# Kernel optimization log

Measured on AMD Instinct MI355X. Metric: run time of the kernel, lower is better.

The kernel has to match this reference:

```python
import jax, jax.numpy as jnp
import numpy as np

EMBED = 1024
HEADS = 16
HEAD_DIM = EMBED // HEADS


def setup_inputs() -> dict:
    key = jax.random.key(0)
    ks = jax.random.split(key, 11)
    B, L, D = 2, 2048, EMBED
    s = 0.02
    return {
        "q": jax.random.normal(ks[0], (B, L, D), jnp.float32),
        "k": jax.random.normal(ks[1], (B, L, D), jnp.float32),
        "v": jax.random.normal(ks[2], (B, L, D), jnp.float32),
        "w_q": jax.random.normal(ks[3], (D, D), jnp.float32) * s,
        "b_q": jnp.zeros((D,), jnp.float32),
        "w_k": jax.random.normal(ks[4], (D, D), jnp.float32) * s,
        "b_k": jnp.zeros((D,), jnp.float32),
        "w_v": jax.random.normal(ks[5], (D, D), jnp.float32) * s,
        "b_v": jnp.zeros((D,), jnp.float32),
        "w_o": jax.random.normal(ks[6], (D, D), jnp.float32) * s,
        "b_o": jnp.zeros((D,), jnp.float32),
    }


def reference(q, k, v, w_q, b_q, w_k, b_k, w_v, b_v, w_o, b_o):
    B, L, D = q.shape
    H, Dh = HEADS, HEAD_DIM
    # Linear projections (torch Linear: x @ W.T + b)
    qp = (q @ w_q.T + b_q).reshape(B, L, H, Dh)
    kp = (k @ w_k.T + b_k).reshape(B, L, H, Dh)
    vp = (v @ w_v.T + b_v).reshape(B, L, H, Dh)
    # energy: [n, h, q, k]
    energy = jnp.einsum("nqhd,nkhd->nhqk", qp, kp)
    scale = 1.0 / jnp.sqrt(jnp.asarray(Dh, qp.dtype))
    attn = jax.nn.softmax(energy * scale, axis=-1)
    ctx = jnp.einsum("nhql,nlhd->nqhd", attn, vp).reshape(B, L, D)
    return ctx @ w_o.T + b_o
```

## Files before the change

### kernel.cpp

```cpp
#include <hip/hip_runtime.h>

typedef __bf16 bf16;
typedef __bf16 bf16x4 __attribute__((ext_vector_type(4)));
typedef __bf16 bf16x8 __attribute__((ext_vector_type(8)));
typedef float f32x4 __attribute__((ext_vector_type(4)));

#define MFMA16(a, b, c) __builtin_amdgcn_mfma_f32_16x16x32_bf16((a), (b), (c), 0, 0, 0)

#define QSCALE 0.18033688011112042f

__device__ inline void gld16(const void* g, void* l) {
    __builtin_amdgcn_global_load_lds(
        (const __attribute__((address_space(1))) unsigned int*)g,
        (__attribute__((address_space(3))) unsigned int*)l, 16, 0, 0);
}

__device__ inline bf16x8 cvt8(float4 a, float4 b) {
    bf16x8 v;
    v[0] = (bf16)a.x; v[1] = (bf16)a.y; v[2] = (bf16)a.z; v[3] = (bf16)a.w;
    v[4] = (bf16)b.x; v[5] = (bf16)b.y; v[6] = (bf16)b.z; v[7] = (bf16)b.w;
    return v;
}

__global__ __launch_bounds__(256) void cvt3_kernel(
    const float* __restrict__ s0, bf16* __restrict__ d0,
    const float* __restrict__ s1, bf16* __restrict__ d1,
    const float* __restrict__ s2, bf16* __restrict__ d2)
{
    const float* src = blockIdx.y == 0 ? s0 : blockIdx.y == 1 ? s1 : s2;
    bf16*        dst = blockIdx.y == 0 ? d0 : blockIdx.y == 1 ? d1 : d2;
    int i = (blockIdx.x * 256 + threadIdx.x) * 8;
    float4 a = *(const float4*)&src[i];
    float4 b = *(const float4*)&src[i + 4];
    *(bf16x8*)&dst[i] = cvt8(a, b);
}

__global__ __launch_bounds__(256) void cvt_kernel(
    const float* __restrict__ src, bf16* __restrict__ dst, int n)
{
    int i = (blockIdx.x * 256 + threadIdx.x) * 8;
    if (i < n) {
        float4 a = *(const float4*)&src[i];
        float4 b = *(const float4*)&src[i + 4];
        *(bf16x8*)&dst[i] = cvt8(a, b);
    }
}

__global__ __launch_bounds__(256) void qkv_gemm(
    const float* __restrict__ q, const float* __restrict__ k,
    const float* __restrict__ v,
    const bf16* __restrict__ wq, const float* __restrict__ bq,
    const bf16* __restrict__ wk, const float* __restrict__ bk,
    const bf16* __restrict__ wv, const float* __restrict__ bv,
    bf16* __restrict__ Qp, bf16* __restrict__ Kp, bf16* __restrict__ Vt)
{
    __shared__ __align__(16) bf16 sm[8192 + 2 * 8192];
    bf16* As = sm;
    bf16* Bs = sm + 8192;
    bf16* Ts = sm;

    const int id  = blockIdx.x;
    const int pr  = (id >> 6) * 8 + (id & 7);
    const int proj = pr >> 5;
    const int m0  = (pr & 31) * 128;
    const int n0  = ((id >> 3) & 7) * 128;

    const float* A    = proj == 0 ? q  : proj == 1 ? k  : v;
    const bf16*  B    = proj == 0 ? wq : proj == 1 ? wk : wv;
    const float* bias = proj == 0 ? bq : proj == 1 ? bk : bv;

    const int tid  = threadIdx.x;
    const int lane = tid & 63;
    const int w    = tid >> 6;
    const int g    = lane >> 4;
    const int ln   = lane & 15;
    const int rowb = (w & 1) * 64;
    const int colb = (w >> 1) * 64;
    const int srow = tid >> 3, slc = tid & 7;
    const int ro   = lane >> 3, lc = lane & 7;

    float4 ra[4][2];
    for (int i = 0; i < 4; ++i) {
        const float* p = &A[(size_t)(m0 + srow + 32 * i) * 1024 + slc * 8];
        ra[i][0] = *(const float4*)p;
        ra[i][1] = *(const float4*)(p + 4);
    }
    for (int j = 0; j < 4; ++j) {
        int base = w * 32 + j * 8;
        int row  = base + ro;
        int c    = lc ^ (row & 7);
        gld16(&B[(size_t)(n0 + row) * 1024 + c * 8], &Bs[base * 64]);
    }

    f32x4 acc[4][4] = {};

    for (int t = 0; t < 16; ++t) {
        __syncthreads();
        for (int i = 0; i < 4; ++i) {
            int row = srow + 32 * i;
            *(bf16x8*)&As[row * 64 + (slc ^ (row & 7)) * 8] = cvt8(ra[i][0], ra[i][1]);
        }
        __syncthreads();
        if (t < 15) {
            int k1 = (t + 1) * 64;
            for (int i = 0; i < 4; ++i) {
                const float* p = &A[(size_t)(m0 + srow + 32 * i) * 1024 + k1 + slc * 8];
                ra[i][0] = *(const float4*)p;
                ra[i][1] = *(const float4*)(p + 4);
            }
            int bsel = (t + 1) & 1;
            for (int j = 0; j < 4; ++j) {
                int base = w * 32 + j * 8;
                int row  = base + ro;
                int c    = lc ^ (row & 7);
                gld16(&B[(size_t)(n0 + row) * 1024 + k1 + c * 8],
                      &Bs[bsel * 8192 + base * 64]);
            }
        }
        const bf16* Bt = Bs + (t & 1) * 8192;
        for (int ks = 0; ks < 2; ++ks) {
            bf16x8 af[4], bfm[4];
            for (int mi = 0; mi < 4; ++mi) {
                int row = rowb + mi * 16 + ln;
                af[mi] = *(const bf16x8*)&As[row * 64 + ((ks * 4 + g) ^ (ln & 7)) * 8];
            }
            for (int ni = 0; ni < 4; ++ni) {
                int row = colb + ni * 16 + ln;
                bfm[ni] = *(const bf16x8*)&Bt[row * 64 + ((ks * 4 + g) ^ (ln & 7)) * 8];
            }
            for (int mi = 0; mi < 4; ++mi)
                for (int ni = 0; ni < 4; ++ni)
                    acc[mi][ni] = MFMA16(af[mi], bfm[ni], acc[mi][ni]);
        }
    }

    if (proj != 2) {
        for (int mi = 0; mi < 4; ++mi) {
            for (int ni = 0; ni < 4; ++ni) {
                int col = n0 + colb + ni * 16 + ln;
                float bv_ = bias[col];
                int rowbase = m0 + rowb + mi * 16 + g * 4;
                if (proj == 0) {
                    for (int r = 0; r < 4; ++r)
                        Qp[(size_t)(rowbase + r) * 1024 + col] =
                            (bf16)((acc[mi][ni][r] + bv_) * QSCALE);
                } else {
                    for (int r = 0; r < 4; ++r)
                        Kp[(size_t)(rowbase + r) * 1024 + col] =
                            (bf16)(acc[mi][ni][r] + bv_);
                }
            }
        }
    } else {
        __syncthreads();
        for (int mi = 0; mi < 4; ++mi) {
            for (int ni = 0; ni < 4; ++ni) {
                int col = colb + ni * 16 + ln;
                float bv_ = bias[n0 + col];
                int row = rowb + mi * 16 + g * 4;
                bf16x4 pk;
                for (int r = 0; r < 4; ++r) pk[r] = (bf16)(acc[mi][ni][r] + bv_);
                *(bf16x4*)&Ts[col * 132 + row] = pk;
            }
        }
        __syncthreads();
        const int bidx = m0 >> 11;
        const int tok0 = m0 & 2047;
        for (int i = 0; i < 8; ++i) {
            int c    = tid + 256 * i;
            int col  = c >> 4;
            int t64  = (c >> 3) & 1;
            int cc   = c & 7;
            int gcol = n0 + col;
            union { bf16 e[8]; uint4 u; } tmp;
            for (int j = 0; j < 8; ++j) {
                int s = 2 * cc + (j >> 2) + ((j & 3) << 4);
                tmp.e[j] = Ts[col * 132 + t64 * 64 + s];
            }
            size_t dst = ((size_t)(bidx * 16 + (gcol >> 6)) * 64 + (gcol & 63)) * 2048
                         + tok0 + t64 * 64 + cc * 8;
            *(uint4*)&Vt[dst] = tmp.u;
        }
    }
}

__global__ __launch_bounds__(256) void gemm_out(
    const bf16* __restrict__ A, const bf16* __restrict__ B,
    const float* __restrict__ bias, float* __restrict__ C)
{
    __shared__ __align__(16) bf16 sm[2 * 4096 + 2 * 8192];
    bf16* As = sm;
    bf16* Bs = sm + 8192;

    const int id = blockIdx.x;
    const int m0 = ((id >> 6) * 8 + (id & 7)) * 64;
    const int n0 = ((id >> 3) & 7) * 128;

    const int tid  = threadIdx.x;
    const int lane = tid & 63;
    const int w    = tid >> 6;
    const int g    = lane >> 4;
    const int ln   = lane & 15;
    const int rowb = (w & 1) * 32;
    const int colb = (w >> 1) * 64;
    const int ro   = lane >> 3, lc = lane & 7;

    auto issue = [&](int t) {
        int k0 = t * 64, sel = t & 1;
        for (int j = 0; j < 2; ++j) {
            int base = w * 16 + j * 8;
            int row  = base + ro;
            int c    = lc ^ (row & 7);
            gld16(&A[(size_t)(m0 + row) * 1024 + k0 + c * 8],
                  &As[sel * 4096 + base * 64]);
        }
        for (int j = 0; j < 4; ++j) {
            int base = w * 32 + j * 8;
            int row  = base + ro;
            int c    = lc ^ (row & 7);
            gld16(&B[(size_t)(n0 + row) * 1024 + k0 + c * 8],
                  &Bs[sel * 8192 + base * 64]);
        }
    };

    issue(0);
    f32x4 acc[2][4] = {};

    for (int t = 0; t < 16; ++t) {
        __syncthreads();
        if (t < 15) issue(t + 1);
        const bf16* At = As + (t & 1) * 4096;
        const bf16* Bt = Bs + (t & 1) * 8192;
        for (int ks = 0; ks < 2; ++ks) {
            bf16x8 af[2], bfm[4];
            for (int mi = 0; mi < 2; ++mi) {
                int row = rowb + mi * 16 + ln;
                af[mi] = *(const bf16x8*)&At[row * 64 + ((ks * 4 + g) ^ (ln & 7)) * 8];
            }
            for (int ni = 0; ni < 4; ++ni) {
                int row = colb + ni * 16 + ln;
                bfm[ni] = *(const bf16x8*)&Bt[row * 64 + ((ks * 4 + g) ^ (ln & 7)) * 8];
            }
            for (int mi = 0; mi < 2; ++mi)
                for (int ni = 0; ni < 4; ++ni)
                    acc[mi][ni] = MFMA16(af[mi], bfm[ni], acc[mi][ni]);
        }
    }

    for (int mi = 0; mi < 2; ++mi) {
        for (int ni = 0; ni < 4; ++ni) {
            int col = n0 + colb + ni * 16 + ln;
            float bv_ = bias[col];
            int rowbase = m0 + rowb + mi * 16 + g * 4;
            for (int r = 0; r < 4; ++r)
                C[(size_t)(rowbase + r) * 1024 + col] = acc[mi][ni][r] + bv_;
        }
    }
}

__global__ __launch_bounds__(256) void attn_kernel(
    const bf16* __restrict__ Qp, const bf16* __restrict__ Kp,
    const bf16* __restrict__ Vt, bf16* __restrict__ Ctx)
{
    __shared__ __align__(16) bf16 smem[8192 + 2 * 4096 + 2 * 4096];
    bf16* Ps = smem;
    bf16* Qs = smem;
    bf16* Ks = smem + 8192;
    bf16* Vs = smem + 16384;

    const int id = blockIdx.x;
    const int qt = (id >> 3) & 15;
    const int bh = (id >> 7) * 8 + (id & 7);

    const int tid  = threadIdx.x;
    const int lane = tid & 63;
    const int w    = tid >> 6;
    const int g    = lane >> 4;
    const int ln   = lane & 15;
    const int ro   = lane >> 3, lc = lane & 7;
    const size_t rowQ0 = (size_t)(bh >> 4) * 2048 + qt * 128;
    const size_t rowK0 = (size_t)(bh >> 4) * 2048;
    const int hcol = (bh & 15) * 64;
    const bf16* VtB = Vt + (size_t)bh * 64 * 2048;

    for (int j = 0; j < 4; ++j) {
        int base = w * 32 + j * 8;
        int row  = base + ro;
        int c    = lc ^ (row & 7);
        gld16(&Qp[(rowQ0 + row) * 1024 + hcol + c * 8], &Qs[base * 64]);
    }
    for (int j = 0; j < 2; ++j) {
        int base = w * 16 + j * 8;
        int kv   = base + ro;
        int c    = lc ^ (kv & 7);
        gld16(&Kp[(rowK0 + kv) * 1024 + hcol + c * 8], &Ks[base * 64]);
        gld16(&VtB[(size_t)kv * 2048 + c * 8], &Vs[base * 64]);
    }
    __syncthreads();

    bf16x8 qf[2][2];
    for (int mi = 0; mi < 2; ++mi)
        for (int ks = 0; ks < 2; ++ks) {
            int row = w * 32 + mi * 16 + ln;
            qf[mi][ks] = *(const bf16x8*)&Qs[row * 64 + ((ks * 4 + g) ^ (ln & 7)) * 8];
        }

    f32x4 oacc[2][4] = {};
    float l_part[2][4] = {};

    for (int t = 0; t < 32; ++t) {
        if (t < 31) {
            int sel = (t + 1) & 1, kvo = (t + 1) * 64;
            for (int j = 0; j < 2; ++j) {
                int base = w * 16 + j * 8;
                int kv   = base + ro;
                int c    = lc ^ (kv & 7);
                gld16(&Kp[(rowK0 + kvo + kv) * 1024 + hcol + c * 8],
                      &Ks[sel * 4096 + base * 64]);
                gld16(&VtB[(size_t)kv * 2048 + kvo + c * 8],
                      &Vs[sel * 4096 + base * 64]);
            }
        }
        const bf16* Kt = Ks + (t & 1) * 4096;
        const bf16* Vti = Vs + (t & 1) * 4096;

        f32x4 sf[2][4] = {};
        for (int ks = 0; ks < 2; ++ks) {
            bf16x8 kf[4];
            for (int nj = 0; nj < 4; ++nj) {
                int row = nj * 16 + ln;
                kf[nj] = *(const bf16x8*)&Kt[row * 64 + ((ks * 4 + g) ^ (ln & 7)) * 8];
            }
            for (int mi = 0; mi < 2; ++mi)
                for (int nj = 0; nj < 4; ++nj)
                    sf[mi][nj] = MFMA16(qf[mi][ks], kf[nj], sf[mi][nj]);
        }

        for (int mi = 0; mi < 2; ++mi) {
            for (int r = 0; r < 4; ++r) {
                float p0 = __builtin_amdgcn_exp2f(sf[mi][0][r]);
                float p1 = __builtin_amdgcn_exp2f(sf[mi][1][r]);
                float p2 = __builtin_amdgcn_exp2f(sf[mi][2][r]);
                float p3 = __builtin_amdgcn_exp2f(sf[mi][3][r]);
                l_part[mi][r] += (p0 + p1) + (p2 + p3);
                int qrow = w * 32 + mi * 16 + g * 4 + r;
                int slot = ln ^ ((qrow & 7) << 1);
                bf16x4 pk;
                pk[0] = (bf16)p0; pk[1] = (bf16)p1; pk[2] = (bf16)p2; pk[3] = (bf16)p3;
                *(bf16x4*)&Ps[qrow * 64 + slot * 4] = pk;
            }
        }

        for (int ks = 0; ks < 2; ++ks) {
            bf16x8 pf[2], vf[4];
            for (int mi = 0; mi < 2; ++mi) {
                int row = w * 32 + mi * 16 + ln;
                int p = (ks * 8 + g * 2) ^ ((row & 7) << 1);
                pf[mi] = *(const bf16x8*)&Ps[row * 64 + p * 4];
            }
            for (int nd = 0; nd < 4; ++nd) {
                int row = nd * 16 + ln;
                vf[nd] = *(const bf16x8*)&Vti[row * 64 + ((ks * 4 + g) ^ (ln & 7)) * 8];
            }
            for (int mi = 0; mi < 2; ++mi)
                for (int nd = 0; nd < 4; ++nd)
                    oacc[mi][nd] = MFMA16(pf[mi], vf[nd], oacc[mi][nd]);
        }
        __syncthreads();
    }

    for (int mi = 0; mi < 2; ++mi) {
        for (int r = 0; r < 4; ++r) {
            float l = l_part[mi][r];
            for (int off = 8; off >= 1; off >>= 1)
                l += __shfl_xor(l, off, 64);
            float inv = 1.0f / l;
            size_t row = rowQ0 + w * 32 + mi * 16 + g * 4 + r;
            for (int nd = 0; nd < 4; ++nd)
                Ctx[row * 1024 + hcol + nd * 16 + ln] = (bf16)(oacc[mi][nd][r] * inv);
        }
    }
}

extern "C" void kernel_launch(void* const* d_in, const int* in_sizes, int n_in,
                              void* d_out, int out_size, void* d_ws, size_t ws_size,
                              hipStream_t stream)
{
    const float* q  = (const float*)d_in[0];
    const float* k  = (const float*)d_in[1];
    const float* v  = (const float*)d_in[2];
    const float* wq = (const float*)d_in[3];
    const float* bq = (const float*)d_in[4];
    const float* wk = (const float*)d_in[5];
    const float* bk = (const float*)d_in[6];
    const float* wv = (const float*)d_in[7];
    const float* bv = (const float*)d_in[8];
    const float* wo = (const float*)d_in[9];
    const float* bo = (const float*)d_in[10];
    float* out = (float*)d_out;

    const int M = 4096, D = 1024;
    bf16* Qp = (bf16*)d_ws;
    bf16* Kp = Qp + (size_t)M * D;
    bf16* Vt = Kp + (size_t)M * D;
    bf16* Ctx = Qp;
    bf16* wob = Kp;

    bf16* wqb = (bf16*)d_out;
    bf16* wkb = wqb + (size_t)D * D;
    bf16* wvb = wkb + (size_t)D * D;

    cvt3_kernel<<<dim3(512, 3), 256, 0, stream>>>(wq, wqb, wk, wkb, wv, wvb);
    qkv_gemm<<<768, 256, 0, stream>>>(q, k, v, wqb, bq, wkb, bk, wvb, bv,
                                      Qp, Kp, Vt);
    attn_kernel<<<512, 256, 0, stream>>>(Qp, Kp, Vt, Ctx);
    cvt_kernel<<<512, 256, 0, stream>>>(wo, wob, D * D);
    gemm_out<<<512, 256, 0, stream>>>(Ctx, wob, bo, out);
}
```

Baseline: 239.0 us.

## Pre-convert activations to bf16, load QKV tiles via LDS DMA, halve attention q-tile

Adds a single conversion kernel that turns q, k, v and all four weights into bf16 up front. A new QKV GEMM can then stream both operands straight into LDS with global_load_lds instead of converting fp32 in registers. The attention kernel now uses 64-row query tiles across 1024 blocks instead of 128-row tiles across 512, for more parallelism and less shared memory per block. The fast path runs only if the workspace is at least 40 MB, otherwise it falls back to the old sequence. The new GEMM drops double-buffering and waits on each stage, and the extra conversion pass adds memory traffic.

```diff
diff --git a/kernel.cpp b/kernel.cpp
--- a/kernel.cpp
+++ b/kernel.cpp
@@ -20,6 +20,33 @@
     v[0] = (bf16)a.x; v[1] = (bf16)a.y; v[2] = (bf16)a.z; v[3] = (bf16)a.w;
     v[4] = (bf16)b.x; v[5] = (bf16)b.y; v[6] = (bf16)b.z; v[7] = (bf16)b.w;
     return v;
+}
+
+__global__ __launch_bounds__(256) void cvt7_kernel(
+    const float* __restrict__ q,  bf16* __restrict__ qb,
+    const float* __restrict__ k,  bf16* __restrict__ kb,
+    const float* __restrict__ v,  bf16* __restrict__ vb,
+    const float* __restrict__ wq, bf16* __restrict__ wqb,
+    const float* __restrict__ wk, bf16* __restrict__ wkb,
+    const float* __restrict__ wv, bf16* __restrict__ wvb,
+    const float* __restrict__ wo, bf16* __restrict__ wob)
+{
+    const float* src; bf16* dst; int n;
+    switch (blockIdx.y) {
+        case 0: src = q;  dst = qb;  n = 1 << 22; break;
+        case 1: src = k;  dst = kb;  n = 1 << 22; break;
+        case 2: src = v;  dst = vb;  n = 1 << 22; break;
+        case 3: src = wq; dst = wqb; n = 1 << 20; break;
+        case 4: src = wk; dst = wkb; n = 1 << 20; break;
+        case 5: src = wv; dst = wvb; n = 1 << 20; break;
+        default: src = wo; dst = wob; n = 1 << 20; break;
+    }
+    int i = (blockIdx.x * 256 + threadIdx.x) * 8;
+    if (i < n) {
+        float4 a = *(const float4*)&src[i];
+        float4 b = *(const float4*)&src[i + 4];
+        *(bf16x8*)&dst[i] = cvt8(a, b);
+    }
 }
 
 __global__ __launch_bounds__(256) void cvt3_kernel(
@@ -46,15 +73,15 @@
     }
 }
 
-__global__ __launch_bounds__(256) void qkv_gemm(
-    const float* __restrict__ q, const float* __restrict__ k,
-    const float* __restrict__ v,
+__global__ __launch_bounds__(256) void qkv_bf16(
+    const bf16* __restrict__ qb, const bf16* __restrict__ kb,
+    const bf16* __restrict__ vb,
     const bf16* __restrict__ wq, const float* __restrict__ bq,
     const bf16* __restrict__ wk, const float* __restrict__ bk,
     const bf16* __restrict__ wv, const float* __restrict__ bv,
     bf16* __restrict__ Qp, bf16* __restrict__ Kp, bf16* __restrict__ Vt)
 {
-    __shared__ __align__(16) bf16 sm[8192 + 2 * 8192];
+    __shared__ __align__(16) bf16 sm[16896];
     bf16* As = sm;
     bf16* Bs = sm + 8192;
     bf16* Ts = sm;
@@ -65,7 +92,7 @@
     const int m0  = (pr & 31) * 128;
     const int n0  = ((id >> 3) & 7) * 128;
 
-    const float* A    = proj == 0 ? q  : proj == 1 ? k  : v;
+    const bf16*  A    = proj == 0 ? qb : proj == 1 ? kb : vb;
     const bf16*  B    = proj == 0 ? wq : proj == 1 ? wk : wv;
     const float* bias = proj == 0 ? bq : proj == 1 ? bk : bv;
 
@@ -76,48 +103,24 @@
     const int ln   = lane & 15;
     const int rowb = (w & 1) * 64;
     const int colb = (w >> 1) * 64;
-    const int srow = tid >> 3, slc = tid & 7;
     const int ro   = lane >> 3, lc = lane & 7;
 
-    float4 ra[4][2];
-    for (int i = 0; i < 4; ++i) {
-        const float* p = &A[(size_t)(m0 + srow + 32 * i) * 1024 + slc * 8];
-        ra[i][0] = *(const float4*)p;
-        ra[i][1] = *(const float4*)(p + 4);
-    }
-    for (int j = 0; j < 4; ++j) {
-        int base = w * 32 + j * 8;
-        int row  = base + ro;
-        int c    = lc ^ (row & 7);
-        gld16(&B[(size_t)(n0 + row) * 1024 + c * 8], &Bs[base * 64]);
-    }
-
+    auto issue = [&](int t) {
+        int k0 = t * 64;
+        for (int j = 0; j < 4; ++j) {
+            int base = w * 32 + j * 8;
+            int row  = base + ro;
+            int c    = lc ^ (row & 7);
+            gld16(&A[(size_t)(m0 + row) * 1024 + k0 + c * 8], &As[base * 64]);
+            gld16(&B[(size_t)(n0 + row) * 1024 + k0 + c * 8], &Bs[base * 64]);
+        }
+    };
+
+    issue(0);
     f32x4 acc[4][4] = {};
 
     for (int t = 0; t < 16; ++t) {
         __syncthreads();
-        for (int i = 0; i < 4; ++i) {
-            int row = srow + 32 * i;
-            *(bf16x8*)&As[row * 64 + (slc ^ (row & 7)) * 8] = cvt8(ra[i][0], ra[i][1]);
-        }
-        __syncthreads();
-        if (t < 15) {
-            int k1 = (t + 1) * 64;
-            for (int i = 0; i < 4; ++i) {
-                const float* p = &A[(size_t)(m0 + srow + 32 * i) * 1024 + k1 + slc * 8];
-                ra[i][0] = *(const float4*)p;
-                ra[i][1] = *(const float4*)(p + 4);
-            }
-            int bsel = (t + 1) & 1;
-            for (int j = 0; j < 4; ++j) {
-                int base = w * 32 + j * 8;
-                int row  = base + ro;
-                int c    = lc ^ (row & 7);
-                gld16(&B[(size_t)(n0 + row) * 1024 + k1 + c * 8],
-                      &Bs[bsel * 8192 + base * 64]);
-            }
-        }
-        const bf16* Bt = Bs + (t & 1) * 8192;
         for (int ks = 0; ks < 2; ++ks) {
             bf16x8 af[4], bfm[4];
             for (int mi = 0; mi < 4; ++mi) {
@@ -126,12 +129,14 @@
             }
             for (int ni = 0; ni < 4; ++ni) {
                 int row = colb + ni * 16 + ln;
-                bfm[ni] = *(const bf16x8*)&Bt[row * 64 + ((ks * 4 + g) ^ (ln & 7)) * 8];
+                bfm[ni] = *(const bf16x8*)&Bs[row * 64 + ((ks * 4 + g) ^ (ln & 7)) * 8];
             }
             for (int mi = 0; mi < 4; ++mi)
                 for (int ni = 0; ni < 4; ++ni)
                     acc[mi][ni] = MFMA16(af[mi], bfm[ni], acc[mi][ni]);
         }
+        __syncthreads();
+        if (t < 15) issue(t + 1);
     }
 
     if (proj != 2) {
@@ -152,7 +157,6 @@
             }
         }
     } else {
-        __syncthreads();
         for (int mi = 0; mi < 4; ++mi) {
             for (int ni = 0; ni < 4; ++ni) {
                 int col = colb + ni * 16 + ln;
@@ -184,6 +188,144 @@
     }
 }
 
+__global__ __launch_bounds__(256) void qkv_gemm(
+    const float* __restrict__ q, const float* __restrict__ k,
+    const float* __restrict__ v,
+    const bf16* __restrict__ wq, const float* __restrict__ bq,
+    const bf16* __restrict__ wk, const float* __restrict__ bk,
+    const bf16* __restrict__ wv, const float* __restrict__ bv,
+    bf16* __restrict__ Qp, bf16* __restrict__ Kp, bf16* __restrict__ Vt)
+{
+    __shared__ __align__(16) bf16 sm[8192 + 2 * 8192];
+    bf16* As = sm;
+    bf16* Bs = sm + 8192;
+    bf16* Ts = sm;
+
+    const int id  = blockIdx.x;
+    const int pr  = (id >> 6) * 8 + (id & 7);
+    const int proj = pr >> 5;
+    const int m0  = (pr & 31) * 128;
+    const int n0  = ((id >> 3) & 7) * 128;
+
+    const float* A    = proj == 0 ? q  : proj == 1 ? k  : v;
+    const bf16*  B    = proj == 0 ? wq : proj == 1 ? wk : wv;
+    const float* bias = proj == 0 ? bq : proj == 1 ? bk : bv;
+
+    const int tid  = threadIdx.x;
+    const int lane = tid & 63;
+    const int w    = tid >> 6;
+    const int g    = lane >> 4;
+    const int ln   = lane & 15;
+    const int rowb = (w & 1) * 64;
+    const int colb = (w >> 1) * 64;
+    const int srow = tid >> 3, slc = tid & 7;
+    const int ro   = lane >> 3, lc = lane & 7;
+
+    float4 ra[4][2];
+    for (int i = 0; i < 4; ++i) {
+        const float* p = &A[(size_t)(m0 + srow + 32 * i) * 1024 + slc * 8];
+        ra[i][0] = *(const float4*)p;
+        ra[i][1] = *(const float4*)(p + 4);
+    }
+    for (int j = 0; j < 4; ++j) {
+        int base = w * 32 + j * 8;
+        int row  = base + ro;
+        int c    = lc ^ (row & 7);
+        gld16(&B[(size_t)(n0 + row) * 1024 + c * 8], &Bs[base * 64]);
+    }
+
+    f32x4 acc[4][4] = {};
+
+    for (int t = 0; t < 16; ++t) {
+        __syncthreads();
+        for (int i = 0; i < 4; ++i) {
+            int row = srow + 32 * i;
+            *(bf16x8*)&As[row * 64 + (slc ^ (row & 7)) * 8] = cvt8(ra[i][0], ra[i][1]);
+        }
+        __syncthreads();
+        if (t < 15) {
+            int k1 = (t + 1) * 64;
+            for (int i = 0; i < 4; ++i) {
+                const float* p = &A[(size_t)(m0 + srow + 32 * i) * 1024 + k1 + slc * 8];
+                ra[i][0] = *(const float4*)p;
+                ra[i][1] = *(const float4*)(p + 4);
+            }
+            int bsel = (t + 1) & 1;
+            for (int j = 0; j < 4; ++j) {
+                int base = w * 32 + j * 8;
+                int row  = base + ro;
+                int c    = lc ^ (row & 7);
+                gld16(&B[(size_t)(n0 + row) * 1024 + k1 + c * 8],
+                      &Bs[bsel * 8192 + base * 64]);
+            }
+        }
+        const bf16* Bt = Bs + (t & 1) * 8192;
+        for (int ks = 0; ks < 2; ++ks) {
+            bf16x8 af[4], bfm[4];
+            for (int mi = 0; mi < 4; ++mi) {
+                int row = rowb + mi * 16 + ln;
+                af[mi] = *(const bf16x8*)&As[row * 64 + ((ks * 4 + g) ^ (ln & 7)) * 8];
+            }
+            for (int ni = 0; ni < 4; ++ni) {
+                int row = colb + ni * 16 + ln;
+                bfm[ni] = *(const bf16x8*)&Bt[row * 64 + ((ks * 4 + g) ^ (ln & 7)) * 8];
+            }
+            for (int mi = 0; mi < 4; ++mi)
+                for (int ni = 0; ni < 4; ++ni)
+                    acc[mi][ni] = MFMA16(af[mi], bfm[ni], acc[mi][ni]);
+        }
+    }
+
+    if (proj != 2) {
+        for (int mi = 0; mi < 4; ++mi) {
+            for (int ni = 0; ni < 4; ++ni) {
+                int col = n0 + colb + ni * 16 + ln;
+                float bv_ = bias[col];
+                int rowbase = m0 + rowb + mi * 16 + g * 4;
+                if (proj == 0) {
+                    for (int r = 0; r < 4; ++r)
+                        Qp[(size_t)(rowbase + r) * 1024 + col] =
+                            (bf16)((acc[mi][ni][r] + bv_) * QSCALE);
+                } else {
+                    for (int r = 0; r < 4; ++r)
+                        Kp[(size_t)(rowbase + r) * 1024 + col] =
+                            (bf16)(acc[mi][ni][r] + bv_);
+                }
+            }
+        }
+    } else {
+        __syncthreads();
+        for (int mi = 0; mi < 4; ++mi) {
+            for (int ni = 0; ni < 4; ++ni) {
+                int col = colb + ni * 16 + ln;
+                float bv_ = bias[n0 + col];
+                int row = rowb + mi * 16 + g * 4;
+                bf16x4 pk;
+                for (int r = 0; r < 4; ++r) pk[r] = (bf16)(acc[mi][ni][r] + bv_);
+                *(bf16x4*)&Ts[col * 132 + row] = pk;
+            }
+        }
+        __syncthreads();
+        const int bidx = m0 >> 11;
+        const int tok0 = m0 & 2047;
+        for (int i = 0; i < 8; ++i) {
+            int c    = tid + 256 * i;
+            int col  = c >> 4;
+            int t64  = (c >> 3) & 1;
+            int cc   = c & 7;
+            int gcol = n0 + col;
+            union { bf16 e[8]; uint4 u; } tmp;
+            for (int j = 0; j < 8; ++j) {
+                int s = 2 * cc + (j >> 2) + ((j & 3) << 4);
+                tmp.e[j] = Ts[col * 132 + t64 * 64 + s];
+            }
+            size_t dst = ((size_t)(bidx * 16 + (gcol >> 6)) * 64 + (gcol & 63)) * 2048
+                         + tok0 + t64 * 64 + cc * 8;
+            *(uint4*)&Vt[dst] = tmp.u;
+        }
+    }
+}
+
 __global__ __launch_bounds__(256) void gemm_out(
     const bf16* __restrict__ A, const bf16* __restrict__ B,
     const float* __restrict__ bias, float* __restrict__ C)
@@ -262,15 +404,15 @@
     const bf16* __restrict__ Qp, const bf16* __restrict__ Kp,
     const bf16* __restrict__ Vt, bf16* __restrict__ Ctx)
 {
-    __shared__ __align__(16) bf16 smem[8192 + 2 * 4096 + 2 * 4096];
+    __shared__ __align__(16) bf16 smem[4096 + 2 * 4096 + 2 * 4096];
     bf16* Ps = smem;
     bf16* Qs = smem;
-    bf16* Ks = smem + 8192;
-    bf16* Vs = smem + 16384;
+    bf16* Ks = smem + 4096;
+    bf16* Vs = smem + 12288;
 
     const int id = blockIdx.x;
-    const int qt = (id >> 3) & 15;
-    const int bh = (id >> 7) * 8 + (id & 7);
+    const int qt = (id >> 3) & 31;
+    const int bh = (id & 7) + ((id >> 8) << 3);
 
     const int tid  = threadIdx.x;
     const int lane = tid & 63;
@@ -278,35 +420,29 @@
     const int g    = lane >> 4;
     const int ln   = lane & 15;
     const int ro   = lane >> 3, lc = lane & 7;
-    const size_t rowQ0 = (size_t)(bh >> 4) * 2048 + qt * 128;
+    const size_t rowQ0 = (size_t)(bh >> 4) * 2048 + qt * 64;
     const size_t rowK0 = (size_t)(bh >> 4) * 2048;
     const int hcol = (bh & 15) * 64;
     const bf16* VtB = Vt + (size_t)bh * 64 * 2048;
 
-    for (int j = 0; j < 4; ++j) {
-        int base = w * 32 + j * 8;
+    for (int j = 0; j < 2; ++j) {
+        int base = w * 16 + j * 8;
         int row  = base + ro;
         int c    = lc ^ (row & 7);
         gld16(&Qp[(rowQ0 + row) * 1024 + hcol + c * 8], &Qs[base * 64]);
-    }
-    for (int j = 0; j < 2; ++j) {
-        int base = w * 16 + j * 8;
-        int kv   = base + ro;
-        int c    = lc ^ (kv & 7);
-        gld16(&Kp[(rowK0 + kv) * 1024 + hcol + c * 8], &Ks[base * 64]);
-        gld16(&VtB[(size_t)kv * 2048 + c * 8], &Vs[base * 64]);
+        gld16(&Kp[(rowK0 + row) * 1024 + hcol + c * 8], &Ks[base * 64]);
+        gld16(&VtB[(size_t)row * 2048 + c * 8], &Vs[base * 64]);
     }
     __syncthreads();
 
-    bf16x8 qf[2][2];
-    for (int mi = 0; mi < 2; ++mi)
-        for (int ks = 0; ks < 2; ++ks) {
-            int row = w * 32 + mi * 16 + ln;
-            qf[mi][ks] = *(const bf16x8*)&Qs[row * 64 + ((ks * 4 + g) ^ (ln & 7)) * 8];
-        }
-
-    f32x4 oacc[2][4] = {};
-    float l_part[2][4] = {};
+    bf16x8 qf[2];
+    for (int ks = 0; ks < 2; ++ks) {
+        int row = w * 16 + ln;
+        qf[ks] = *(const bf16x8*)&Qs[row * 64 + ((ks * 4 + g) ^ (ln & 7)) * 8];
+    }
+
+    f32x4 oacc[4] = {};
+    float l_part[4] = {};
 
     for (int t = 0; t < 32; ++t) {
         if (t < 31) {
@@ -321,64 +457,58 @@
                       &Vs[sel * 4096 + base * 64]);
             }
         }
-        const bf16* Kt = Ks + (t & 1) * 4096;
+        const bf16* Kt  = Ks + (t & 1) * 4096;
         const bf16* Vti = Vs + (t & 1) * 4096;
 
-        f32x4 sf[2][4] = {};
+        f32x4 sf[4] = {};
         for (int ks = 0; ks < 2; ++ks) {
             bf16x8 kf[4];
             for (int nj = 0; nj < 4; ++nj) {
                 int row = nj * 16 + ln;
                 kf[nj] = *(const bf16x8*)&Kt[row * 64 + ((ks * 4 + g) ^ (ln & 7)) * 8];
             }
-            for (int mi = 0; mi < 2; ++mi)
-                for (int nj = 0; nj < 4; ++nj)
-                    sf[mi][nj] = MFMA16(qf[mi][ks], kf[nj], sf[mi][nj]);
-        }
-
-        for (int mi = 0; mi < 2; ++mi) {
-            for (int r = 0; r < 4; ++r) {
-                float p0 = __builtin_amdgcn_exp2f(sf[mi][0][r]);
-                float p1 = __builtin_amdgcn_exp2f(sf[mi][1][r]);
-                float p2 = __builtin_amdgcn_exp2f(sf[mi][2][r]);
-                float p3 = __builtin_amdgcn_exp2f(sf[mi][3][r]);
-                l_part[mi][r] += (p0 + p1) + (p2 + p3);
-                int qrow = w * 32 + mi * 16 + g * 4 + r;
-                int slot = ln ^ ((qrow & 7) << 1);
-                bf16x4 pk;
-                pk[0] = (bf16)p0; pk[1] = (bf16)p1; pk[2] = (bf16)p2; pk[3] = (bf16)p3;
-                *(bf16x4*)&Ps[qrow * 64 + slot * 4] = pk;
-            }
+            for (int nj = 0; nj < 4; ++nj)
+                sf[nj] = MFMA16(qf[ks], kf[nj], sf[nj]);
+        }
+
+        for (int r = 0; r < 4; ++r) {
+            float p0 = __builtin_amdgcn_exp2f(sf[0][r]);
+            float p1 = __builtin_amdgcn_exp2f(sf[1][r]);
+            float p2 = __builtin_amdgcn_exp2f(sf[2][r]);
+            float p3 = __builtin_amdgcn_exp2f(sf[3][r]);
+            l_part[r] += (p0 + p1) + (p2 + p3);
+            int qrow = w * 16 + g * 4 + r;
+            int slot = ln ^ ((qrow & 7) << 1);
+            bf16x4 pk;
+            pk[0] = (bf16)p0; pk[1] = (bf16)p1; pk[2] = (bf16)p2; pk[3] = (bf16)p3;
+            *(bf16x4*)&Ps[qrow * 64 + slot * 4] = pk;
         }
 
         for (int ks = 0; ks < 2; ++ks) {
-            bf16x8 pf[2], vf[4];
-            for (int mi = 0; mi < 2; ++mi) {
-                int row = w * 32 + mi * 16 + ln;
+            bf16x8 pf, vf[4];
+            {
+                int row = w * 16 + ln;
                 int p = (ks * 8 + g * 2) ^ ((row & 7) << 1);
-                pf[mi] = *(const bf16x8*)&Ps[row * 64 + p * 4];
+                pf = *(const bf16x8*)&Ps[row * 64 + p * 4];
             }
             for (int nd = 0; nd < 4; ++nd) {
                 int row = nd * 16 + ln;
                 vf[nd] = *(const bf16x8*)&Vti[row * 64 + ((ks * 4 + g) ^ (ln & 7)) * 8];
             }
-            for (int mi = 0; mi < 2; ++mi)
-                for (int nd = 0; nd < 4; ++nd)
-                    oacc[mi][nd] = MFMA16(pf[mi], vf[nd], oacc[mi][nd]);
-        }
-        __syncthreads();
-    }
-
-    for (int mi = 0; mi < 2; ++mi) {
-        for (int r = 0; r < 4; ++r) {
-            float l = l_part[mi][r];
-            for (int off = 8; off >= 1; off >>= 1)
-                l += __shfl_xor(l, off, 64);
-            float inv = 1.0f / l;
-            size_t row = rowQ0 + w * 32 + mi * 16 + g * 4 + r;
             for (int nd = 0; nd < 4; ++nd)
-                Ctx[row * 1024 + hcol + nd * 16 + ln] = (bf16)(oacc[mi][nd][r] * inv);
-        }
+                oacc[nd] = MFMA16(pf, vf[nd], oacc[nd]);
+        }
+        __syncthreads();
+    }
+
+    for (int r = 0; r < 4; ++r) {
+        float l = l_part[r];
+        for (int off = 8; off >= 1; off >>= 1)
+            l += __shfl_xor(l, off, 64);
+        float inv = 1.0f / l;
+        size_t row = rowQ0 + w * 16 + g * 4 + r;
+        for (int nd = 0; nd < 4; ++nd)
+            Ctx[row * 1024 + hcol + nd * 16 + ln] = (bf16)(oacc[nd][r] * inv);
     }
 }
 
@@ -399,21 +529,39 @@
     const float* bo = (const float*)d_in[10];
     float* out = (float*)d_out;
 
-    const int M = 4096, D = 1024;
-    bf16* Qp = (bf16*)d_ws;
-    bf16* Kp = Qp + (size_t)M * D;
-    bf16* Vt = Kp + (size_t)M * D;
+    const int D = 1024;
+    bf16* W  = (bf16*)d_ws;
+    bf16* Qp = W;
+    bf16* Kp = W + (1u << 22);
+    bf16* Vt = W + (2u << 22);
     bf16* Ctx = Qp;
-    bf16* wob = Kp;
-
-    bf16* wqb = (bf16*)d_out;
-    bf16* wkb = wqb + (size_t)D * D;
-    bf16* wvb = wkb + (size_t)D * D;
-
-    cvt3_kernel<<<dim3(512, 3), 256, 0, stream>>>(wq, wqb, wk, wkb, wv, wvb);
-    qkv_gemm<<<768, 256, 0, stream>>>(q, k, v, wqb, bq, wkb, bk, wvb, bv,
-                                      Qp, Kp, Vt);
-    attn_kernel<<<512, 256, 0, stream>>>(Qp, Kp, Vt, Ctx);
-    cvt_kernel<<<512, 256, 0, stream>>>(wo, wob, D * D);
-    gemm_out<<<512, 256, 0, stream>>>(Ctx, wob, bo, out);
-}
+
+    if (ws_size >= (size_t)40 * 1024 * 1024) {
+        bf16* vb  = W + (3u << 22);
+        bf16* wqb = W + (1u << 24);
+        bf16* wkb = wqb + (1u << 20);
+        bf16* wvb = wkb + (1u << 20);
+        bf16* wob = wvb + (1u << 20);
+        bf16* qb  = (bf16*)d_out;
+        bf16* kb  = qb + (1u << 22);
+
+        cvt7_kernel<<<dim3(2048, 7), 256, 0, stream>>>(
+            q, qb, k, kb, v, vb, wq, wqb, wk, wkb, wv, wvb, wo, wob);
+        qkv_bf16<<<768, 256, 0, stream>>>(qb, kb, vb, wqb, bq, wkb, bk, wvb, bv,
+                                          Qp, Kp, Vt);
+        attn_kernel<<<1024, 256, 0, stream>>>(Qp, Kp, Vt, Ctx);
+        gemm_out<<<512, 256, 0, stream>>>(Ctx, wob, bo, out);
+    } else {
+        bf16* wqb = (bf16*)d_out;
+        bf16* wkb = wqb + (size_t)D * D;
+        bf16* wvb = wkb + (size_t)D * D;
+        bf16* wob = Kp;
+
+        cvt3_kernel<<<dim3(512, 3), 256, 0, stream>>>(wq, wqb, wk, wkb, wv, wvb);
+        qkv_gemm<<<768, 256, 0, stream>>>(q, k, v, wqb, bq, wkb, bk, wvb, bv,
+                                          Qp, Kp, Vt);
+        attn_kernel<<<1024, 256, 0, stream>>>(Qp, Kp, Vt, Ctx);
+        cvt_kernel<<<512, 256, 0, stream>>>(wo, wob, D * D);
+        gemm_out<<<512, 256, 0, stream>>>(Ctx, wob, bo, out);
+    }
+}
```

Result: faster. 224.2 us (-6.2%).
